# Kernel tuning notes

Hardware: AMD Instinct MI355X
Metric: run time of the kernel (lower is better)

The kernel has to match this reference:

```python
import jax, jax.numpy as jnp
import numpy as np

EPS = 1e-06


def setup_inputs() -> dict:
    key = jax.random.key(0)
    kq, kk, kv = jax.random.split(key, 3)
    B, H, T, P = 2, 8, 1024, 64
    Q = jax.random.normal(kq, (B, H, T, P), dtype=jnp.float32)
    K = jax.random.normal(kk, (B, H, T, P), dtype=jnp.float32)
    V = jax.random.normal(kv, (B, H, T, P), dtype=jnp.float32)
    return {"Q": Q, "K": K, "V": V}


def _scan_attention(Q, K, V):
    Q_feat = jnp.exp(Q)                                  # (B,H,T,P)
    K_feat = jnp.exp(K)                                  # (B,H,T,P)
    m0 = jnp.log(K_feat)                                 # (B,H,T,P)
    N0 = jnp.einsum('bhtp,bhtn->bhtpn', V, K_feat)       # (B,H,T,P,P) matrix state
    D0 = K_feat                                          # (B,H,T,P)

    def combine(x, y):
        m_x, N_x, D_x = x
        m_y, N_y, D_y = y
        m_new = jnp.maximum(m_x, m_y)
        scale_x = jnp.exp(m_x - m_new)
        scale_y = jnp.exp(m_y - m_new)
        N_new = N_x * scale_x[..., None] + N_y * scale_y[..., None]
        D_new = D_x * scale_x + D_y * scale_y
        return (m_new, N_new, D_new)

    m_cum, num_cum, denom_cum = jax.lax.associative_scan(combine, (m0, N0, D0), axis=2)

    Y_num = jnp.einsum('bhtp,bhtpq->bhtq', Q_feat, num_cum)   # (B,H,T,P)
    Y_den = jnp.einsum('bhtp,bhtp->bht', Q_feat, denom_cum)   # (B,H,T)
    Y = Y_num / (Y_den[..., None] + EPS)
    B, H, T, P = Q.shape
    return Y.transpose(0, 2, 1, 3).reshape(B, T, H * P)


def reference(Q, K, V):
    return _scan_attention(Q, K, V)
```

## Files before the change

### kernel.cpp

```cpp
#include <hip/hip_runtime.h>
#include <hip/hip_bf16.h>

#define TDIM 1024
#define PDIM 64
#define BHN  16
#define NCH  64
#define CHS  16

typedef __bf16 bf16_t;
typedef bf16_t bf16x8 __attribute__((ext_vector_type(8)));
typedef float  floatx4 __attribute__((ext_vector_type(4)));

__device__ __forceinline__ floatx4 mfma16(bf16x8 a, bf16x8 b, floatx4 c) {
    return __builtin_amdgcn_mfma_f32_16x16x32_bf16(a, b, c, 0, 0, 0);
}

__global__ __launch_bounds__(64) void stats_kernel(
        const float* __restrict__ K,
        float* __restrict__ cmax, float* __restrict__ csum) {
    int bh = blockIdx.x >> 6;
    int c  = blockIdx.x & 63;
    int p  = threadIdx.x;
    const float* Kb = K + (size_t)bh * TDIM * PDIM + (size_t)c * CHS * PDIM + p;
    float k[CHS];
#pragma unroll
    for (int i = 0; i < CHS; ++i) k[i] = Kb[i * PDIM];
    float m = -INFINITY, s = 0.f;
#pragma unroll
    for (int i = 0; i < CHS; ++i) {
        m = fmaxf(m, k[i]);
        float e = __expf(k[i]);
        s += e * e;
    }
    cmax[(bh * NCH + c) * PDIM + p] = m;
    csum[(bh * NCH + c) * PDIM + p] = s;
}

__global__ __launch_bounds__(64) void feat_kernel(
        const float* __restrict__ Q, const float* __restrict__ K,
        const float* __restrict__ V,
        const float* __restrict__ cmax, const float* __restrict__ csum,
        bf16_t* __restrict__ W, bf16_t* __restrict__ U,
        bf16_t* __restrict__ Kft, float* __restrict__ den) {
    int bh = blockIdx.x >> 6;
    int c  = blockIdx.x & 63;
    int p  = threadIdx.x;
    size_t base = (size_t)bh * TDIM * PDIM;
    int t0 = c * CHS;

    float m = -INFINITY, s = 0.f;
#pragma unroll 8
    for (int cc = 0; cc < c; ++cc) {
        m = fmaxf(m, cmax[(bh * NCH + cc) * PDIM + p]);
        s += csum[(bh * NCH + cc) * PDIM + p];
    }

    float kq[CHS], qq_[CHS], vv[CHS];
#pragma unroll
    for (int i = 0; i < CHS; ++i) {
        kq[i]  = K[base + (size_t)(t0 + i) * PDIM + p];
        qq_[i] = Q[base + (size_t)(t0 + i) * PDIM + p];
        vv[i]  = V[base + (size_t)(t0 + i) * PDIM + p];
    }

    __shared__ bf16_t ek_t[CHS][PDIM + 4];
    __shared__ float  dt[CHS][PDIM + 1];

#pragma unroll
    for (int i = 0; i < CHS; ++i) {
        int t = t0 + i;
        m = fmaxf(m, kq[i]);
        float ek = __expf(kq[i]);
        s += ek * ek;
        float w = __expf(qq_[i] - m);
        W[base + (size_t)t * PDIM + p] = (bf16_t)w;
        U[base + (size_t)t * PDIM + p] = (bf16_t)(vv[i] * ek);
        ek_t[i][p] = (bf16_t)ek;
        dt[i][p] = w * s;
    }
    __syncthreads();

    {
        int tl = p >> 2, g = p & 3;
        float d = 0.f;
#pragma unroll
        for (int i = 0; i < 16; ++i) d += dt[tl][i * 4 + g];
        d += __shfl_xor(d, 1);
        d += __shfl_xor(d, 2);
        if (g == 0) den[bh * TDIM + t0 + tl] = d;
    }

    {
        int hi = p >> 4, tl = p & 15;
#pragma unroll
        for (int it = 0; it < 16; ++it) {
            int q = it * 4 + hi;
            Kft[((size_t)bh * PDIM + q) * TDIM + t0 + tl] = ek_t[tl][q];
        }
    }
}

__global__ __launch_bounds__(512) void attn_kernel(
        const bf16_t* __restrict__ W, const bf16_t* __restrict__ U,
        const bf16_t* __restrict__ Kft, const float* __restrict__ den,
        float* __restrict__ out) {
    int bh  = blockIdx.x & 15;
    int i   = blockIdx.x >> 4;
    int tid = threadIdx.x;
    int wave = tid >> 6, lane = tid & 63;
    int lq = lane & 15, qd = lane >> 4;
    int sub = wave & 3;
    int par = wave >> 2;
    int b = bh >> 3, h = bh & 7;

    __shared__ bf16_t Ct[8][16][72];
    __shared__ float  Yred[4][16][68];
    __shared__ float  denb[64];

    size_t base = (size_t)bh * TDIM * PDIM;
    int trow0 = i * 64 + sub * 16;

    if (tid < 64) denb[tid] = den[bh * TDIM + i * 64 + tid];

    const bf16_t* wrow = W + base + (size_t)(trow0 + lq) * PDIM;
    bf16x8 a0 = *(const bf16x8*)(wrow + qd * 8);
    bf16x8 a1 = *(const bf16x8*)(wrow + 32 + qd * 8);

    floatx4 acc[4];
#pragma unroll
    for (int j = 0; j < 4; ++j) acc[j] = (floatx4){0.f, 0.f, 0.f, 0.f};

    for (int kt = par; kt <= i; kt += 2) {
        bf16x8 ub[8], kb[8];
        const bf16_t* ubase = U + base + (size_t)(kt * 64) * PDIM;
        const bf16_t* kbase = Kft + (size_t)bh * PDIM * TDIM + kt * 64;
#pragma unroll
        for (int j = 0; j < 4; ++j) {
            const bf16_t* ur = ubase + (size_t)(j * 16 + lq) * PDIM;
            ub[2 * j]     = *(const bf16x8*)(ur + qd * 8);
            ub[2 * j + 1] = *(const bf16x8*)(ur + 32 + qd * 8);
        }
#pragma unroll
        for (int j = 0; j < 4; ++j) {
            const bf16_t* kr = kbase + (size_t)(j * 16 + lq) * TDIM;
            kb[2 * j]     = *(const bf16x8*)(kr + qd * 8);
            kb[2 * j + 1] = *(const bf16x8*)(kr + 32 + qd * 8);
        }

        floatx4 cc[4];
#pragma unroll
        for (int j = 0; j < 4; ++j) {
            floatx4 t = (floatx4){0.f, 0.f, 0.f, 0.f};
            t = mfma16(a0, ub[2 * j], t);
            t = mfma16(a1, ub[2 * j + 1], t);
            cc[j] = t;
        }

#pragma unroll
        for (int j = 0; j < 4; ++j) {
#pragma unroll
            for (int r = 0; r < 4; ++r) {
                float v = cc[j][r];
                if (kt == i && (kt * 64 + j * 16 + lq) > (trow0 + qd * 4 + r))
                    v = 0.f;
                Ct[wave][qd * 4 + r][j * 16 + lq] = (bf16_t)v;
            }
        }

        bf16x8 ca0 = *(const bf16x8*)&Ct[wave][lq][qd * 8];
        bf16x8 ca1 = *(const bf16x8*)&Ct[wave][lq][32 + qd * 8];
#pragma unroll
        for (int j = 0; j < 4; ++j) {
            acc[j] = mfma16(ca0, kb[2 * j], acc[j]);
            acc[j] = mfma16(ca1, kb[2 * j + 1], acc[j]);
        }
    }

    if (par == 1) {
#pragma unroll
        for (int j = 0; j < 4; ++j)
#pragma unroll
            for (int r = 0; r < 4; ++r)
                Yred[sub][qd * 4 + r][j * 16 + lq] = acc[j][r];
    }
    __syncthreads();
    if (par == 0) {
#pragma unroll
        for (int j = 0; j < 4; ++j) {
#pragma unroll
            for (int r = 0; r < 4; ++r) {
                int trow_l = sub * 16 + qd * 4 + r;
                int tg = i * 64 + trow_l;
                float y = acc[j][r] + Yred[sub][qd * 4 + r][j * 16 + lq];
                y = y / (denb[trow_l] + 1e-6f);
                out[((size_t)b * TDIM + tg) * (8 * PDIM) + h * PDIM + j * 16 + lq] = y;
            }
        }
    }
}

extern "C" void kernel_launch(void* const* d_in, const int* in_sizes, int n_in,
                              void* d_out, int out_size, void* d_ws, size_t ws_size,
                              hipStream_t stream) {
    const float* Q = (const float*)d_in[0];
    const float* K = (const float*)d_in[1];
    const float* V = (const float*)d_in[2];
    float* out = (float*)d_out;

    bf16_t* Wf   = (bf16_t*)d_ws;
    bf16_t* Uf   = Wf + (size_t)BHN * TDIM * PDIM;
    bf16_t* Kft  = Uf + (size_t)BHN * TDIM * PDIM;
    float*  den  = (float*)(Kft + (size_t)BHN * TDIM * PDIM);
    float*  cmax = den + (size_t)BHN * TDIM;
    float*  csum = cmax + (size_t)BHN * NCH * PDIM;

    stats_kernel<<<BHN * NCH, 64, 0, stream>>>(K, cmax, csum);
    feat_kernel<<<BHN * NCH, 64, 0, stream>>>(Q, K, V, cmax, csum, Wf, Uf, Kft, den);
    attn_kernel<<<256, 512, 0, stream>>>(Wf, Uf, Kft, den, out);
}
```

Baseline: 103.1 us.

## Stage U and K tiles through shared memory with register prefetch in attention kernel

The attention kernel now loads each 64x64 U and transposed-K tile cooperatively into LDS once per block, instead of having every wave fetch its own copies from global memory. The next pair of tiles is prefetched into registers while the current pair is being computed, to overlap global loads with MFMA work. The Ct and Yred scratch buffers now share one LDS region. In exchange the kernel adds two block-wide barriers per iteration and uses more LDS, which may reduce occupancy.

```diff
diff --git a/kernel.cpp b/kernel.cpp
--- a/kernel.cpp
+++ b/kernel.cpp
@@ -113,69 +113,87 @@
     int par = wave >> 2;
     int b = bh >> 3, h = bh & 7;
 
-    __shared__ bf16_t Ct[8][16][72];
-    __shared__ float  Yred[4][16][68];
-    __shared__ float  denb[64];
+    __shared__ bf16_t Wt[64][72];
+    __shared__ bf16_t Ut[2][64][72];
+    __shared__ bf16_t Kt[2][64][72];
+    __shared__ __align__(16) char ctyraw[8 * 16 * 72 * 2];
+    __shared__ float denb[64];
+    bf16_t (*Ct)[16][72]  = (bf16_t (*)[16][72])ctyraw;
+    float  (*Yred)[16][68] = (float (*)[16][68])ctyraw;
 
     size_t base = (size_t)bh * TDIM * PDIM;
-    int trow0 = i * 64 + sub * 16;
-
+    size_t kftb = (size_t)bh * PDIM * TDIM;
+    int row = tid >> 3, c8 = (tid & 7) << 3;
+
+    int4 wfrag = *(const int4*)(W + base + (size_t)(i * 64 + row) * PDIM + c8);
+    int4 pu0 = *(const int4*)(U + base + (size_t)(0 * 64 + row) * PDIM + c8);
+    int4 pk0 = *(const int4*)(Kft + kftb + (size_t)row * TDIM + 0 * 64 + c8);
+    int4 pu1 = *(const int4*)(U + base + (size_t)(1 * 64 + row) * PDIM + c8);
+    int4 pk1 = *(const int4*)(Kft + kftb + (size_t)row * TDIM + 1 * 64 + c8);
+    *(int4*)&Wt[row][c8] = wfrag;
     if (tid < 64) denb[tid] = den[bh * TDIM + i * 64 + tid];
-
-    const bf16_t* wrow = W + base + (size_t)(trow0 + lq) * PDIM;
-    bf16x8 a0 = *(const bf16x8*)(wrow + qd * 8);
-    bf16x8 a1 = *(const bf16x8*)(wrow + 32 + qd * 8);
+    __syncthreads();
+
+    bf16x8 a0 = *(const bf16x8*)&Wt[sub * 16 + lq][qd * 8];
+    bf16x8 a1 = *(const bf16x8*)&Wt[sub * 16 + lq][32 + qd * 8];
 
     floatx4 acc[4];
 #pragma unroll
     for (int j = 0; j < 4; ++j) acc[j] = (floatx4){0.f, 0.f, 0.f, 0.f};
 
-    for (int kt = par; kt <= i; kt += 2) {
-        bf16x8 ub[8], kb[8];
-        const bf16_t* ubase = U + base + (size_t)(kt * 64) * PDIM;
-        const bf16_t* kbase = Kft + (size_t)bh * PDIM * TDIM + kt * 64;
-#pragma unroll
-        for (int j = 0; j < 4; ++j) {
-            const bf16_t* ur = ubase + (size_t)(j * 16 + lq) * PDIM;
-            ub[2 * j]     = *(const bf16x8*)(ur + qd * 8);
-            ub[2 * j + 1] = *(const bf16x8*)(ur + 32 + qd * 8);
-        }
-#pragma unroll
-        for (int j = 0; j < 4; ++j) {
-            const bf16_t* kr = kbase + (size_t)(j * 16 + lq) * TDIM;
-            kb[2 * j]     = *(const bf16x8*)(kr + qd * 8);
-            kb[2 * j + 1] = *(const bf16x8*)(kr + 32 + qd * 8);
-        }
-
-        floatx4 cc[4];
-#pragma unroll
-        for (int j = 0; j < 4; ++j) {
-            floatx4 t = (floatx4){0.f, 0.f, 0.f, 0.f};
-            t = mfma16(a0, ub[2 * j], t);
-            t = mfma16(a1, ub[2 * j + 1], t);
-            cc[j] = t;
-        }
-
-#pragma unroll
-        for (int j = 0; j < 4; ++j) {
-#pragma unroll
-            for (int r = 0; r < 4; ++r) {
-                float v = cc[j][r];
-                if (kt == i && (kt * 64 + j * 16 + lq) > (trow0 + qd * 4 + r))
-                    v = 0.f;
-                Ct[wave][qd * 4 + r][j * 16 + lq] = (bf16_t)v;
-            }
-        }
-
-        bf16x8 ca0 = *(const bf16x8*)&Ct[wave][lq][qd * 8];
-        bf16x8 ca1 = *(const bf16x8*)&Ct[wave][lq][32 + qd * 8];
-#pragma unroll
-        for (int j = 0; j < 4; ++j) {
-            acc[j] = mfma16(ca0, kb[2 * j], acc[j]);
-            acc[j] = mfma16(ca1, kb[2 * j + 1], acc[j]);
-        }
-    }
-
+    int niter = (i >> 1) + 1;
+    for (int kt2 = 0; kt2 < niter; ++kt2) {
+        __syncthreads();
+        *(int4*)&Ut[0][row][c8] = pu0;
+        *(int4*)&Kt[0][row][c8] = pk0;
+        *(int4*)&Ut[1][row][c8] = pu1;
+        *(int4*)&Kt[1][row][c8] = pk1;
+        if (kt2 + 1 < niter) {
+            int ktn = 2 * kt2 + 2;
+            int ktn1 = ktn + 1 > 15 ? 15 : ktn + 1;
+            pu0 = *(const int4*)(U + base + (size_t)(ktn * 64 + row) * PDIM + c8);
+            pk0 = *(const int4*)(Kft + kftb + (size_t)row * TDIM + ktn * 64 + c8);
+            pu1 = *(const int4*)(U + base + (size_t)(ktn1 * 64 + row) * PDIM + c8);
+            pk1 = *(const int4*)(Kft + kftb + (size_t)row * TDIM + ktn1 * 64 + c8);
+        }
+        __syncthreads();
+
+        int kt = 2 * kt2 + par;
+        if (kt <= i) {
+            floatx4 cc[4];
+#pragma unroll
+            for (int j = 0; j < 4; ++j) {
+                bf16x8 b0 = *(const bf16x8*)&Ut[par][j * 16 + lq][qd * 8];
+                bf16x8 b1 = *(const bf16x8*)&Ut[par][j * 16 + lq][32 + qd * 8];
+                floatx4 t = (floatx4){0.f, 0.f, 0.f, 0.f};
+                t = mfma16(a0, b0, t);
+                t = mfma16(a1, b1, t);
+                cc[j] = t;
+            }
+            int trow0 = i * 64 + sub * 16;
+#pragma unroll
+            for (int j = 0; j < 4; ++j) {
+#pragma unroll
+                for (int r = 0; r < 4; ++r) {
+                    float v = cc[j][r];
+                    if (kt == i && (kt * 64 + j * 16 + lq) > (trow0 + qd * 4 + r))
+                        v = 0.f;
+                    Ct[wave][qd * 4 + r][j * 16 + lq] = (bf16_t)v;
+                }
+            }
+            bf16x8 ca0 = *(const bf16x8*)&Ct[wave][lq][qd * 8];
+            bf16x8 ca1 = *(const bf16x8*)&Ct[wave][lq][32 + qd * 8];
+#pragma unroll
+            for (int j = 0; j < 4; ++j) {
+                bf16x8 kb0 = *(const bf16x8*)&Kt[par][j * 16 + lq][qd * 8];
+                bf16x8 kb1 = *(const bf16x8*)&Kt[par][j * 16 + lq][32 + qd * 8];
+                acc[j] = mfma16(ca0, kb0, acc[j]);
+                acc[j] = mfma16(ca1, kb1, acc[j]);
+            }
+        }
+    }
+
+    __syncthreads();
     if (par == 1) {
 #pragma unroll
         for (int j = 0; j < 4; ++j)
```

Result: faster. 85.29 us (-17.2%).
